# Optimization experiments

Hardware: AMD Instinct MI355X
Metric: run time of the kernel (lower is better)

Reference implementation:

```python
import jax, jax.numpy as jnp
import numpy as np

EPS = 0.1  # eps added to covariance sums, as in torch cov()
N, D, N_CLASSES = 4096, 1024, 64


def setup_inputs() -> dict:
    key = jax.random.key(0)
    k1, k2 = jax.random.split(key)
    inputs = jax.random.normal(k1, (N, D), dtype=jnp.float32)
    targets = jax.random.randint(k2, (N,), 0, N_CLASSES, dtype=jnp.int32)
    return {"inputs": inputs, "targets": targets}


def _masked_sqdiff_sum(M, x):
    # Per-dim sum over masked pairs (i,j) of (x_i - x_j)^2, without
    # materializing the [n, n, d] difference tensor:
    #   sum_ij M_ij (x_id^2 + x_jd^2 - 2 x_id x_jd)
    row = M.sum(axis=1)  # [n]
    col = M.sum(axis=0)  # [n]
    x2 = x * x
    return row @ x2 + col @ x2 - 2.0 * jnp.sum(x * (M @ x), axis=0)  # [d]


def _jeffrey_loss(inputs, targets):
    n = inputs.shape[0]
    same = targets[:, None] == targets[None, :]
    eye = jnp.eye(n, dtype=bool)
    pos_m = (same & ~eye).astype(inputs.dtype)  # positive pairs, i != j
    neg_m = (~same).astype(inputs.dtype)        # negative pairs

    # Covariances are computed on detached diffs in the torch code
    xd = jax.lax.stop_gradient(inputs)
    cnt_pos = pos_m.sum()
    cnt_neg = neg_m.sum()
    sigma1 = (_masked_sqdiff_sum(pos_m, xd) + EPS) / cnt_pos  # [d]
    sigma0 = (_masked_sqdiff_sum(neg_m, xd) + EPS) / cnt_neg  # [d]
    weights = 1.0 / sigma0 - 1.0 / sigma1  # [d], constant w.r.t. grad

    # S[i, j] = sum_d weights_d * (x_i - x_j)_d^2, via gram expansion
    xw = inputs * weights            # [n, d]
    sq = jnp.sum(inputs * xw, axis=1)  # [n], sum_d w_d x_d^2
    S = sq[:, None] + sq[None, :] - 2.0 * inputs @ xw.T  # [n, n]

    # BCEWithLogitsLoss(mean): label 1 on positive pairs (logits a),
    # label 0 on negative pairs (logits b)
    loss_sum = jnp.sum(pos_m * jax.nn.softplus(-S)) + jnp.sum(neg_m * jax.nn.softplus(S))
    return loss_sum / (cnt_pos + cnt_neg)


def reference(inputs, targets):
    return _jeffrey_loss(inputs, targets)
```

## Files before the change

kernel.cpp:

```cpp
#include <hip/hip_runtime.h>
#include <stdint.h>

#define N_ROWS 4096
#define DIM    1024
#define NCLS   64
#define EPSV   0.1f

typedef __attribute__((ext_vector_type(4))) float f32x4;

__device__ __forceinline__ void async_cp16(const void* g, void* l) {
    __builtin_amdgcn_global_load_lds((const __attribute__((address_space(1))) void*)g,
                                     (__attribute__((address_space(3))) void*)l,
                                     16, 0, 0);
}

__device__ __forceinline__ float softplus(float x) {
    return fmaxf(x, 0.f) + __logf(1.f + __expf(-fabsf(x)));
}

__global__ __launch_bounds__(256) void k_cstats(const float* __restrict__ X,
                                                const int* __restrict__ tgt,
                                                float* __restrict__ csumR,
                                                float* __restrict__ csqR) {
    __shared__ int rows[N_ROWS];
    __shared__ int nrows_s;
    int tid = threadIdx.x;
    int c = blockIdx.x >> 2, q = blockIdx.x & 3;
    if (tid == 0) nrows_s = 0;
    __syncthreads();
    for (int i = tid; i < N_ROWS; i += 256)
        if (tgt[i] == c) { int p = atomicAdd(&nrows_s, 1); rows[p] = i; }
    __syncthreads();
    int n = nrows_s;
    int d = q * 256 + tid;
    float s = 0.f, qq = 0.f;
    #pragma unroll 4
    for (int r = 0; r < n; r++) {
        float x = X[(size_t)rows[r] * DIM + d];
        s += x; qq += x * x;
    }
    csumR[c * DIM + d] = s;
    csqR [c * DIM + d] = qq;
}

__global__ __launch_bounds__(1024) void k_weights(const int* __restrict__ tgt,
                                                  const float* __restrict__ csumR,
                                                  const float* __restrict__ csqR,
                                                  float* __restrict__ w,
                                                  float* __restrict__ scal,
                                                  float* __restrict__ loss_out) {
    __shared__ int hist[NCLS];
    __shared__ float redw[16];
    int tid = threadIdx.x;
    if (tid < NCLS) hist[tid] = 0;
    __syncthreads();
    for (int i = tid; i < N_ROWS; i += 1024) atomicAdd(&hist[tgt[i]], 1);
    __syncthreads();
    long long sp = 0, ss = 0;
    for (int c = 0; c < NCLS; c++) { long long cc = hist[c]; sp += cc * (cc - 1); ss += cc * cc; }
    float cnt_pos = (float)sp;
    float cnt_neg = (float)((long long)N_ROWS * N_ROWS - ss);
    int d = tid;
    float A = 0.f, X2 = 0.f, T = 0.f, SS = 0.f;
    #pragma unroll 8
    for (int c = 0; c < NCLS; c++) {
        float s = csumR[c * DIM + d];
        float q = csqR [c * DIM + d];
        A += (float)hist[c] * q; X2 += q; T += s; SS += s * s;
    }
    float posnum = 2.f * (A - SS);
    float negnum = 2.f * ((float)N_ROWS * X2 - A - T * T + SS);
    float wd = cnt_neg / (negnum + EPSV) - cnt_pos / (posnum + EPSV);
    w[d] = wd;
    float m = wd * wd;
    for (int off = 32; off; off >>= 1) m += __shfl_down(m, off, 64);
    int wv = tid >> 6, ln = tid & 63;
    if (ln == 0) redw[wv] = m;
    __syncthreads();
    if (tid == 0) {
        float ms = 0.f;
        #pragma unroll
        for (int i = 0; i < 16; i++) ms += redw[i];
        ms /= 1024.f;
        float sw = exp2f(roundf(log2f(sqrtf(ms) + 1e-30f)));
        scal[0] = sw;
        loss_out[0] = 0.0f;
    }
}

__global__ __launch_bounds__(256) void k_prep(const float* __restrict__ X,
                                              const float* __restrict__ w,
                                              const float* __restrict__ scal,
                                              unsigned int* __restrict__ Xb8,
                                              unsigned int* __restrict__ XWb8,
                                              float* __restrict__ sq) {
    int row = blockIdx.x, tid = threadIdx.x;
    float inv_sw = 1.0f / scal[0];
    float4 x  = ((const float4*)(X + (size_t)row * DIM))[tid];
    float4 ww = ((const float4*)w)[tid];
    float4 xw = make_float4(x.x * ww.x, x.y * ww.y, x.z * ww.z, x.w * ww.w);
    float p = x.x * xw.x + x.y * xw.y + x.z * xw.z + x.w * xw.w;
    unsigned ux = __builtin_amdgcn_cvt_pk_fp8_f32(x.x, x.y, 0, false);
    ux = __builtin_amdgcn_cvt_pk_fp8_f32(x.z, x.w, ux, true);
    unsigned uw = __builtin_amdgcn_cvt_pk_fp8_f32(xw.x * inv_sw, xw.y * inv_sw, 0, false);
    uw = __builtin_amdgcn_cvt_pk_fp8_f32(xw.z * inv_sw, xw.w * inv_sw, uw, true);
    Xb8 [row * 256 + tid] = ux;
    XWb8[row * 256 + tid] = uw;
    for (int off = 32; off; off >>= 1) p += __shfl_down(p, off, 64);
    __shared__ float red[4];
    int wv = tid >> 6, ln = tid & 63;
    if (ln == 0) red[wv] = p;
    __syncthreads();
    if (tid == 0) sq[row] = red[0] + red[1] + red[2] + red[3];
}

__global__ __launch_bounds__(512) void k_gemm_loss(const unsigned char* __restrict__ Xb8,
                                                   const unsigned char* __restrict__ XWb8,
                                                   const float* __restrict__ sq,
                                                   const int* __restrict__ tgt,
                                                   const float* __restrict__ scal,
                                                   float* __restrict__ loss) {
    __shared__ __align__(16) unsigned char As[4][128 * 32];
    __shared__ __align__(16) unsigned char Bs[4][128 * 32];
    __shared__ float sqI[128], sqJ[128];
    __shared__ int   tIs[128], tJs[128];
    __shared__ float red[8];

    int tid = threadIdx.x;
    int wave = tid >> 6, lane = tid & 63;

    int g = blockIdx.x & 7, s = blockIdx.x >> 3;
    int j0 = g, j1 = 15 - g, j2 = 16 + g, j3 = 31 - g;
    int n0 = j0 + 1, n1 = j1 + 1, n2 = j2 + 1;
    int jt, it;
    if      (s < n0)           { jt = j0; it = s; }
    else if (s < n0 + n1)      { jt = j1; it = s - n0; }
    else if (s < n0 + n1 + n2) { jt = j2; it = s - n0 - n1; }
    else                       { jt = j3; it = s - n0 - n1 - n2; }

    bool isA = wave < 4;
    int gIa = wave & 3;
    int r_loc = gIa * 32 + (lane >> 1);
    int swb = ((r_loc >> 1) ^ (r_loc >> 2)) & 1;
    int h_src = (lane & 1) ^ swb;
    int grow = (isA ? it : jt) * 128 + r_loc;
    const unsigned char* gp = (isA ? Xb8 : XWb8) + (size_t)grow * DIM + h_src * 16;
    unsigned char* lbase = (isA ? &As[0][0] : &Bs[0][0]) + gIa * 1024;

    int lr = lane & 15, kq = lane >> 4;
    int offA[4], offB[2];
    int wrow = (wave >> 2) * 64, wcol = (wave & 3) * 32;
    #pragma unroll
    for (int mi = 0; mi < 4; mi++) {
        int row = wrow + mi * 16 + lr;
        offA[mi] = row * 32 + ((kq ^ ((((row >> 1) ^ (row >> 2)) & 1) << 1)) * 8);
    }
    #pragma unroll
    for (int nj = 0; nj < 2; nj++) {
        int col = wcol + nj * 16 + lr;
        offB[nj] = col * 32 + ((kq ^ ((((col >> 1) ^ (col >> 2)) & 1) << 1)) * 8);
    }

    f32x4 acc[4][2];
    #pragma unroll
    for (int i = 0; i < 4; i++)
        #pragma unroll
        for (int j = 0; j < 2; j++) acc[i][j] = (f32x4){0.f, 0.f, 0.f, 0.f};

    #pragma unroll
    for (int st = 0; st < 3; st++) async_cp16(gp + st * 32, lbase + st * (128 * 32));

    for (int kk = 0; kk < 32; kk++) {
        if      (kk < 30)  asm volatile("s_waitcnt vmcnt(2)" ::: "memory");
        else if (kk == 30) asm volatile("s_waitcnt vmcnt(1)" ::: "memory");
        else               asm volatile("s_waitcnt vmcnt(0)" ::: "memory");
        asm volatile("s_barrier" ::: "memory");
        if (kk < 29) {
            async_cp16(gp + (kk + 3) * 32, lbase + ((kk + 3) & 3) * (128 * 32));
        }
        int rd = kk & 3;
        const unsigned char* Ab = As[rd];
        const unsigned char* Bb = Bs[rd];
        long long av[4], bv[2];
        #pragma unroll
        for (int i = 0; i < 4; i++) av[i] = *(const long long*)(Ab + offA[i]);
        #pragma unroll
        for (int j = 0; j < 2; j++) bv[j] = *(const long long*)(Bb + offB[j]);
        #pragma unroll
        for (int i = 0; i < 4; i++)
            #pragma unroll
            for (int j = 0; j < 2; j++)
                acc[i][j] = __builtin_amdgcn_mfma_f32_16x16x32_fp8_fp8(av[i], bv[j], acc[i][j], 0, 0, 0);
    }

    __syncthreads();
    if (tid < 128)      { sqI[tid] = sq[it * 128 + tid]; tIs[tid] = tgt[it * 128 + tid]; }
    else if (tid < 256) { int u = tid - 128; sqJ[u] = sq[jt * 128 + u]; tJs[u] = tgt[jt * 128 + u]; }
    __syncthreads();

    float sw2 = 2.0f * scal[0];
    float sum = 0.f;
    bool diagTile = (it == jt);
    #pragma unroll
    for (int j = 0; j < 2; j++) {
        int col = wcol + j * 16 + (lane & 15);
        float sj = sqJ[col]; int tj = tJs[col];
        #pragma unroll
        for (int i = 0; i < 4; i++) {
            int rbase = wrow + i * 16 + (lane >> 4) * 4;
            #pragma unroll
            for (int r = 0; r < 4; r++) {
                int rowp = rbase + r;
                float S = sqI[rowp] + sj - sw2 * acc[i][j][r];
                float v;
                if (tIs[rowp] == tj) v = (diagTile && rowp == col) ? 0.f : softplus(-S);
                else                 v = softplus(S);
                sum += v;
            }
        }
    }
    float scale = (diagTile ? 1.f : 2.f) * (1.f / ((float)N_ROWS * (float)(N_ROWS - 1)));
    sum *= scale;
    for (int off = 32; off; off >>= 1) sum += __shfl_down(sum, off, 64);
    if (lane == 0) red[wave] = sum;
    __syncthreads();
    if (tid == 0) {
        float t = 0.f;
        #pragma unroll
        for (int wv = 0; wv < 8; wv++) t += red[wv];
        atomicAdd(loss, t);
    }
}

extern "C" void kernel_launch(void* const* d_in, const int* in_sizes, int n_in,
                              void* d_out, int out_size, void* d_ws, size_t ws_size,
                              hipStream_t stream) {
    const float* X  = (const float*)d_in[0];
    const int* tgt  = (const int*)d_in[1];
    float* out = (float*)d_out;
    char* ws = (char*)d_ws;
    const size_t MB = 1u << 20;

    float* w      = (float*)ws;
    float* sq     = (float*)(ws + 4096);
    float* scal   = (float*)(ws + 24576);
    unsigned int* Xb8  = (unsigned int*)(ws + 1 * MB);
    unsigned int* XWb8 = (unsigned int*)(ws + 5 * MB);
    float* csumR  = (float*)(ws + 9 * MB);
    float* csqR   = (float*)(ws + 9 * MB + 256 * 1024);

    k_cstats  <<<256,  256, 0, stream>>>(X, tgt, csumR, csqR);
    k_weights <<<1,   1024, 0, stream>>>(tgt, csumR, csqR, w, scal, out);
    k_prep    <<<4096, 256, 0, stream>>>(X, w, scal, Xb8, XWb8, sq);
    k_gemm_loss<<<528, 512, 0, stream>>>((const unsigned char*)Xb8, (const unsigned char*)XWb8,
                                         sq, tgt, scal, out);
}
```

Baseline: 125.2 us.

## Enlarge per-wave GEMM tile to 64x64 with 256-thread blocks; split weights kernel

The fused fp8 GEMM+loss kernel now runs 4 waves per block instead of 8. Each wave computes a 64x64 sub-tile (4x4 MFMAs), so each LDS fragment load is reused across more MFMAs, and each thread issues two async global-to-LDS copies per stage. The weights kernel is spread over 8 blocks of 128 threads instead of one block of 1024 threads. The fp8 scale factor is now estimated from only the first 128 weight dimensions, which can slightly change the fp8 quantisation range. The GEMM change also raises accumulator register pressure, which may lower occupancy.

```diff
diff --git a/kernel.cpp b/kernel.cpp
--- a/kernel.cpp
+++ b/kernel.cpp
@@ -43,24 +43,24 @@
     csqR [c * DIM + d] = qq;
 }
 
-__global__ __launch_bounds__(1024) void k_weights(const int* __restrict__ tgt,
-                                                  const float* __restrict__ csumR,
-                                                  const float* __restrict__ csqR,
-                                                  float* __restrict__ w,
-                                                  float* __restrict__ scal,
-                                                  float* __restrict__ loss_out) {
+__global__ __launch_bounds__(128) void k_weights(const int* __restrict__ tgt,
+                                                 const float* __restrict__ csumR,
+                                                 const float* __restrict__ csqR,
+                                                 float* __restrict__ w,
+                                                 float* __restrict__ scal,
+                                                 float* __restrict__ loss_out) {
     __shared__ int hist[NCLS];
-    __shared__ float redw[16];
-    int tid = threadIdx.x;
+    __shared__ float redw[2];
+    int tid = threadIdx.x, b = blockIdx.x;
     if (tid < NCLS) hist[tid] = 0;
     __syncthreads();
-    for (int i = tid; i < N_ROWS; i += 1024) atomicAdd(&hist[tgt[i]], 1);
+    for (int i = tid; i < N_ROWS; i += 128) atomicAdd(&hist[tgt[i]], 1);
     __syncthreads();
     long long sp = 0, ss = 0;
     for (int c = 0; c < NCLS; c++) { long long cc = hist[c]; sp += cc * (cc - 1); ss += cc * cc; }
     float cnt_pos = (float)sp;
     float cnt_neg = (float)((long long)N_ROWS * N_ROWS - ss);
-    int d = tid;
+    int d = b * 128 + tid;
     float A = 0.f, X2 = 0.f, T = 0.f, SS = 0.f;
     #pragma unroll 8
     for (int c = 0; c < NCLS; c++) {
@@ -77,13 +77,9 @@
     int wv = tid >> 6, ln = tid & 63;
     if (ln == 0) redw[wv] = m;
     __syncthreads();
-    if (tid == 0) {
-        float ms = 0.f;
-        #pragma unroll
-        for (int i = 0; i < 16; i++) ms += redw[i];
-        ms /= 1024.f;
-        float sw = exp2f(roundf(log2f(sqrtf(ms) + 1e-30f)));
-        scal[0] = sw;
+    if (b == 0 && tid == 0) {
+        float ms = (redw[0] + redw[1]) / 128.f;
+        scal[0] = exp2f(roundf(log2f(sqrtf(ms) + 1e-30f)));
         loss_out[0] = 0.0f;
     }
 }
@@ -114,7 +110,7 @@
     if (tid == 0) sq[row] = red[0] + red[1] + red[2] + red[3];
 }
 
-__global__ __launch_bounds__(512) void k_gemm_loss(const unsigned char* __restrict__ Xb8,
+__global__ __launch_bounds__(256) void k_gemm_loss(const unsigned char* __restrict__ Xb8,
                                                    const unsigned char* __restrict__ XWb8,
                                                    const float* __restrict__ sq,
                                                    const int* __restrict__ tgt,
@@ -124,7 +120,7 @@
     __shared__ __align__(16) unsigned char Bs[4][128 * 32];
     __shared__ float sqI[128], sqJ[128];
     __shared__ int   tIs[128], tJs[128];
-    __shared__ float red[8];
+    __shared__ float red[4];
 
     int tid = threadIdx.x;
     int wave = tid >> 6, lane = tid & 63;
@@ -138,71 +134,81 @@
     else if (s < n0 + n1 + n2) { jt = j2; it = s - n0 - n1; }
     else                       { jt = j3; it = s - n0 - n1 - n2; }
 
-    bool isA = wave < 4;
-    int gIa = wave & 3;
-    int r_loc = gIa * 32 + (lane >> 1);
-    int swb = ((r_loc >> 1) ^ (r_loc >> 2)) & 1;
-    int h_src = (lane & 1) ^ swb;
-    int grow = (isA ? it : jt) * 128 + r_loc;
-    const unsigned char* gp = (isA ? Xb8 : XWb8) + (size_t)grow * DIM + h_src * 16;
-    unsigned char* lbase = (isA ? &As[0][0] : &Bs[0][0]) + gIa * 1024;
+    bool isA = wave < 2;
+    const unsigned char* srcb = (isA ? Xb8 : XWb8) + (size_t)((isA ? it : jt) * 128) * DIM;
+    unsigned char* slab = isA ? &As[0][0] : &Bs[0][0];
+    const unsigned char* gp[2];
+    unsigned char* lb[2];
+    #pragma unroll
+    for (int si = 0; si < 2; si++) {
+        int chunk = (wave & 1) * 128 + si * 64 + lane;
+        int r = chunk >> 1, h = chunk & 1;
+        int swb = ((r >> 1) ^ (r >> 2)) & 1;
+        gp[si] = srcb + (size_t)r * DIM + (h ^ swb) * 16;
+        lb[si] = slab + ((wave & 1) * 128 + si * 64) * 16;
+    }
 
     int lr = lane & 15, kq = lane >> 4;
-    int offA[4], offB[2];
-    int wrow = (wave >> 2) * 64, wcol = (wave & 3) * 32;
+    int offA[4], offB[4];
+    int wrow = (wave >> 1) * 64, wcol = (wave & 1) * 64;
     #pragma unroll
     for (int mi = 0; mi < 4; mi++) {
         int row = wrow + mi * 16 + lr;
-        offA[mi] = row * 32 + ((kq ^ ((((row >> 1) ^ (row >> 2)) & 1) << 1)) * 8);
-    }
-    #pragma unroll
-    for (int nj = 0; nj < 2; nj++) {
-        int col = wcol + nj * 16 + lr;
-        offB[nj] = col * 32 + ((kq ^ ((((col >> 1) ^ (col >> 2)) & 1) << 1)) * 8);
-    }
-
-    f32x4 acc[4][2];
+        int sw = ((row >> 1) ^ (row >> 2)) & 1;
+        offA[mi] = row * 32 + (kq ^ (sw << 1)) * 8;
+        int col = wcol + mi * 16 + lr;
+        int swc = ((col >> 1) ^ (col >> 2)) & 1;
+        offB[mi] = col * 32 + (kq ^ (swc << 1)) * 8;
+    }
+
+    f32x4 acc[4][4];
     #pragma unroll
     for (int i = 0; i < 4; i++)
         #pragma unroll
-        for (int j = 0; j < 2; j++) acc[i][j] = (f32x4){0.f, 0.f, 0.f, 0.f};
-
-    #pragma unroll
-    for (int st = 0; st < 3; st++) async_cp16(gp + st * 32, lbase + st * (128 * 32));
+        for (int j = 0; j < 4; j++) acc[i][j] = (f32x4){0.f, 0.f, 0.f, 0.f};
+
+    #pragma unroll
+    for (int st = 0; st < 3; st++)
+        #pragma unroll
+        for (int si = 0; si < 2; si++)
+            async_cp16(gp[si] + st * 32, lb[si] + st * 4096);
 
     for (int kk = 0; kk < 32; kk++) {
-        if      (kk < 30)  asm volatile("s_waitcnt vmcnt(2)" ::: "memory");
-        else if (kk == 30) asm volatile("s_waitcnt vmcnt(1)" ::: "memory");
+        if      (kk < 30)  asm volatile("s_waitcnt vmcnt(4)" ::: "memory");
+        else if (kk == 30) asm volatile("s_waitcnt vmcnt(2)" ::: "memory");
         else               asm volatile("s_waitcnt vmcnt(0)" ::: "memory");
         asm volatile("s_barrier" ::: "memory");
         if (kk < 29) {
-            async_cp16(gp + (kk + 3) * 32, lbase + ((kk + 3) & 3) * (128 * 32));
+            #pragma unroll
+            for (int si = 0; si < 2; si++)
+                async_cp16(gp[si] + (kk + 3) * 32, lb[si] + ((kk + 3) & 3) * 4096);
         }
         int rd = kk & 3;
         const unsigned char* Ab = As[rd];
         const unsigned char* Bb = Bs[rd];
-        long long av[4], bv[2];
-        #pragma unroll
-        for (int i = 0; i < 4; i++) av[i] = *(const long long*)(Ab + offA[i]);
-        #pragma unroll
-        for (int j = 0; j < 2; j++) bv[j] = *(const long long*)(Bb + offB[j]);
+        long long av[4], bv[4];
+        #pragma unroll
+        for (int i = 0; i < 4; i++) {
+            av[i] = *(const long long*)(Ab + offA[i]);
+            bv[i] = *(const long long*)(Bb + offB[i]);
+        }
         #pragma unroll
         for (int i = 0; i < 4; i++)
             #pragma unroll
-            for (int j = 0; j < 2; j++)
+            for (int j = 0; j < 4; j++)
                 acc[i][j] = __builtin_amdgcn_mfma_f32_16x16x32_fp8_fp8(av[i], bv[j], acc[i][j], 0, 0, 0);
     }
 
     __syncthreads();
-    if (tid < 128)      { sqI[tid] = sq[it * 128 + tid]; tIs[tid] = tgt[it * 128 + tid]; }
-    else if (tid < 256) { int u = tid - 128; sqJ[u] = sq[jt * 128 + u]; tJs[u] = tgt[jt * 128 + u]; }
+    if (tid < 128) { sqI[tid] = sq[it * 128 + tid]; tIs[tid] = tgt[it * 128 + tid]; }
+    else { int u = tid - 128; sqJ[u] = sq[jt * 128 + u]; tJs[u] = tgt[jt * 128 + u]; }
     __syncthreads();
 
     float sw2 = 2.0f * scal[0];
     float sum = 0.f;
     bool diagTile = (it == jt);
     #pragma unroll
-    for (int j = 0; j < 2; j++) {
+    for (int j = 0; j < 4; j++) {
         int col = wcol + j * 16 + (lane & 15);
         float sj = sqJ[col]; int tj = tJs[col];
         #pragma unroll
@@ -224,12 +230,7 @@
     for (int off = 32; off; off >>= 1) sum += __shfl_down(sum, off, 64);
     if (lane == 0) red[wave] = sum;
     __syncthreads();
-    if (tid == 0) {
-        float t = 0.f;
-        #pragma unroll
-        for (int wv = 0; wv < 8; wv++) t += red[wv];
-        atomicAdd(loss, t);
-    }
+    if (tid == 0) atomicAdd(loss, red[0] + red[1] + red[2] + red[3]);
 }
 
 extern "C" void kernel_launch(void* const* d_in, const int* in_sizes, int n_in,
@@ -250,8 +251,8 @@
     float* csqR   = (float*)(ws + 9 * MB + 256 * 1024);
 
     k_cstats  <<<256,  256, 0, stream>>>(X, tgt, csumR, csqR);
-    k_weights <<<1,   1024, 0, stream>>>(tgt, csumR, csqR, w, scal, out);
+    k_weights <<<8,    128, 0, stream>>>(tgt, csumR, csqR, w, scal, out);
     k_prep    <<<4096, 256, 0, stream>>>(X, w, scal, Xb8, XWb8, sq);
-    k_gemm_loss<<<528, 512, 0, stream>>>((const unsigned char*)Xb8, (const unsigned char*)XWb8,
+    k_gemm_loss<<<528, 256, 0, stream>>>((const unsigned char*)Xb8, (const unsigned char*)XWb8,
                                          sq, tgt, scal, out);
 }
```

New measurement: 130.8 us. +4.4%, slower.

## Pre-swizzle fp8 operands in global memory, split weights kernel across blocks

Applied to the files above, without the earlier changes.

The prep kernel now writes the fp8 X and XW rows in an XOR-swizzled chunk order, so the GEMM kernel can copy 16-byte chunks linearly into LDS and use a wider 2-bit XOR swizzle for its fragment reads, reducing LDS bank conflicts. The weights kernel is split from one 1024-thread block into 8 blocks of 128 threads. The scale factor is now computed from only block 0's 128 weights instead of all 1024, which changes the fp8 scaling and may alter accuracy. The GEMM kernel also gets an occupancy hint in its launch bounds.

```diff
diff --git a/kernel.cpp b/kernel.cpp
--- a/kernel.cpp
+++ b/kernel.cpp
@@ -43,24 +43,24 @@
     csqR [c * DIM + d] = qq;
 }
 
-__global__ __launch_bounds__(1024) void k_weights(const int* __restrict__ tgt,
-                                                  const float* __restrict__ csumR,
-                                                  const float* __restrict__ csqR,
-                                                  float* __restrict__ w,
-                                                  float* __restrict__ scal,
-                                                  float* __restrict__ loss_out) {
+__global__ __launch_bounds__(128) void k_weights(const int* __restrict__ tgt,
+                                                 const float* __restrict__ csumR,
+                                                 const float* __restrict__ csqR,
+                                                 float* __restrict__ w,
+                                                 float* __restrict__ scal,
+                                                 float* __restrict__ loss_out) {
     __shared__ int hist[NCLS];
-    __shared__ float redw[16];
-    int tid = threadIdx.x;
+    __shared__ float redw[2];
+    int tid = threadIdx.x, b = blockIdx.x;
     if (tid < NCLS) hist[tid] = 0;
     __syncthreads();
-    for (int i = tid; i < N_ROWS; i += 1024) atomicAdd(&hist[tgt[i]], 1);
+    for (int i = tid; i < N_ROWS; i += 128) atomicAdd(&hist[tgt[i]], 1);
     __syncthreads();
     long long sp = 0, ss = 0;
     for (int c = 0; c < NCLS; c++) { long long cc = hist[c]; sp += cc * (cc - 1); ss += cc * cc; }
     float cnt_pos = (float)sp;
     float cnt_neg = (float)((long long)N_ROWS * N_ROWS - ss);
-    int d = tid;
+    int d = b * 128 + tid;
     float A = 0.f, X2 = 0.f, T = 0.f, SS = 0.f;
     #pragma unroll 8
     for (int c = 0; c < NCLS; c++) {
@@ -77,13 +77,9 @@
     int wv = tid >> 6, ln = tid & 63;
     if (ln == 0) redw[wv] = m;
     __syncthreads();
-    if (tid == 0) {
-        float ms = 0.f;
-        #pragma unroll
-        for (int i = 0; i < 16; i++) ms += redw[i];
-        ms /= 1024.f;
-        float sw = exp2f(roundf(log2f(sqrtf(ms) + 1e-30f)));
-        scal[0] = sw;
+    if (b == 0 && tid == 0) {
+        float ms = (redw[0] + redw[1]) / 128.f;
+        scal[0] = exp2f(roundf(log2f(sqrtf(ms) + 1e-30f)));
         loss_out[0] = 0.0f;
     }
 }
@@ -104,8 +100,11 @@
     ux = __builtin_amdgcn_cvt_pk_fp8_f32(x.z, x.w, ux, true);
     unsigned uw = __builtin_amdgcn_cvt_pk_fp8_f32(xw.x * inv_sw, xw.y * inv_sw, 0, false);
     uw = __builtin_amdgcn_cvt_pk_fp8_f32(xw.z * inv_sw, xw.w * inv_sw, uw, true);
-    Xb8 [row * 256 + tid] = ux;
-    XWb8[row * 256 + tid] = uw;
+    int t = tid >> 3, q = (tid >> 1) & 3, o = tid & 1;
+    int s = (row >> 2) & 3;
+    int widx = row * 256 + t * 8 + (q ^ s) * 2 + o;
+    Xb8 [widx] = ux;
+    XWb8[widx] = uw;
     for (int off = 32; off; off >>= 1) p += __shfl_down(p, off, 64);
     __shared__ float red[4];
     int wv = tid >> 6, ln = tid & 63;
@@ -114,14 +113,14 @@
     if (tid == 0) sq[row] = red[0] + red[1] + red[2] + red[3];
 }
 
-__global__ __launch_bounds__(512) void k_gemm_loss(const unsigned char* __restrict__ Xb8,
-                                                   const unsigned char* __restrict__ XWb8,
-                                                   const float* __restrict__ sq,
-                                                   const int* __restrict__ tgt,
-                                                   const float* __restrict__ scal,
-                                                   float* __restrict__ loss) {
-    __shared__ __align__(16) unsigned char As[4][128 * 32];
-    __shared__ __align__(16) unsigned char Bs[4][128 * 32];
+__global__ __launch_bounds__(512, 4) void k_gemm_loss(const unsigned char* __restrict__ Xb8,
+                                                      const unsigned char* __restrict__ XWb8,
+                                                      const float* __restrict__ sq,
+                                                      const int* __restrict__ tgt,
+                                                      const float* __restrict__ scal,
+                                                      float* __restrict__ loss) {
+    __shared__ __align__(16) unsigned char As[4][4096];
+    __shared__ __align__(16) unsigned char Bs[4][4096];
     __shared__ float sqI[128], sqJ[128];
     __shared__ int   tIs[128], tJs[128];
     __shared__ float red[8];
@@ -130,22 +129,21 @@
     int wave = tid >> 6, lane = tid & 63;
 
     int g = blockIdx.x & 7, s = blockIdx.x >> 3;
-    int j0 = g, j1 = 15 - g, j2 = 16 + g, j3 = 31 - g;
+    int j0 = g, j1 = 15 - g, j2 = 16 + g;
     int n0 = j0 + 1, n1 = j1 + 1, n2 = j2 + 1;
     int jt, it;
     if      (s < n0)           { jt = j0; it = s; }
     else if (s < n0 + n1)      { jt = j1; it = s - n0; }
     else if (s < n0 + n1 + n2) { jt = j2; it = s - n0 - n1; }
-    else                       { jt = j3; it = s - n0 - n1 - n2; }
+    else                       { jt = 31 - g; it = s - n0 - n1 - n2; }
 
     bool isA = wave < 4;
-    int gIa = wave & 3;
-    int r_loc = gIa * 32 + (lane >> 1);
-    int swb = ((r_loc >> 1) ^ (r_loc >> 2)) & 1;
-    int h_src = (lane & 1) ^ swb;
-    int grow = (isA ? it : jt) * 128 + r_loc;
-    const unsigned char* gp = (isA ? Xb8 : XWb8) + (size_t)grow * DIM + h_src * 16;
-    unsigned char* lbase = (isA ? &As[0][0] : &Bs[0][0]) + gIa * 1024;
+    const unsigned char* srcb = (isA ? Xb8 : XWb8) + (size_t)((isA ? it : jt) * 128) * DIM;
+    unsigned char* slab = isA ? &As[0][0] : &Bs[0][0];
+    int ch = (wave & 3) * 64 + lane;
+    int r = ch >> 1, h = ch & 1;
+    const unsigned char* gp = srcb + (size_t)r * DIM + h * 16;
+    unsigned char* lb = slab + (wave & 3) * 1024;
 
     int lr = lane & 15, kq = lane >> 4;
     int offA[4], offB[2];
@@ -153,12 +151,12 @@
     #pragma unroll
     for (int mi = 0; mi < 4; mi++) {
         int row = wrow + mi * 16 + lr;
-        offA[mi] = row * 32 + ((kq ^ ((((row >> 1) ^ (row >> 2)) & 1) << 1)) * 8);
+        offA[mi] = row * 32 + (kq ^ ((row >> 2) & 3)) * 8;
     }
     #pragma unroll
     for (int nj = 0; nj < 2; nj++) {
         int col = wcol + nj * 16 + lr;
-        offB[nj] = col * 32 + ((kq ^ ((((col >> 1) ^ (col >> 2)) & 1) << 1)) * 8);
+        offB[nj] = col * 32 + (kq ^ ((col >> 2) & 3)) * 8;
     }
 
     f32x4 acc[4][2];
@@ -168,16 +166,15 @@
         for (int j = 0; j < 2; j++) acc[i][j] = (f32x4){0.f, 0.f, 0.f, 0.f};
 
     #pragma unroll
-    for (int st = 0; st < 3; st++) async_cp16(gp + st * 32, lbase + st * (128 * 32));
+    for (int st = 0; st < 3; st++) async_cp16(gp + st * 32, lb + st * 4096);
 
     for (int kk = 0; kk < 32; kk++) {
         if      (kk < 30)  asm volatile("s_waitcnt vmcnt(2)" ::: "memory");
         else if (kk == 30) asm volatile("s_waitcnt vmcnt(1)" ::: "memory");
         else               asm volatile("s_waitcnt vmcnt(0)" ::: "memory");
         asm volatile("s_barrier" ::: "memory");
-        if (kk < 29) {
-            async_cp16(gp + (kk + 3) * 32, lbase + ((kk + 3) & 3) * (128 * 32));
-        }
+        if (kk < 29)
+            async_cp16(gp + (kk + 3) * 32, lb + ((kk + 3) & 3) * 4096);
         int rd = kk & 3;
         const unsigned char* Ab = As[rd];
         const unsigned char* Bb = Bs[rd];
@@ -209,9 +206,9 @@
         for (int i = 0; i < 4; i++) {
             int rbase = wrow + i * 16 + (lane >> 4) * 4;
             #pragma unroll
-            for (int r = 0; r < 4; r++) {
-                int rowp = rbase + r;
-                float S = sqI[rowp] + sj - sw2 * acc[i][j][r];
+            for (int rr = 0; rr < 4; rr++) {
+                int rowp = rbase + rr;
+                float S = sqI[rowp] + sj - sw2 * acc[i][j][rr];
                 float v;
                 if (tIs[rowp] == tj) v = (diagTile && rowp == col) ? 0.f : softplus(-S);
                 else                 v = softplus(S);
@@ -250,7 +247,7 @@
     float* csqR   = (float*)(ws + 9 * MB + 256 * 1024);
 
     k_cstats  <<<256,  256, 0, stream>>>(X, tgt, csumR, csqR);
-    k_weights <<<1,   1024, 0, stream>>>(tgt, csumR, csqR, w, scal, out);
+    k_weights <<<8,    128, 0, stream>>>(tgt, csumR, csqR, w, scal, out);
     k_prep    <<<4096, 256, 0, stream>>>(X, w, scal, Xb8, XWb8, sq);
     k_gemm_loss<<<528, 512, 0, stream>>>((const unsigned char*)Xb8, (const unsigned char*)XWb8,
                                          sq, tgt, scal, out);
```

Result: faster. 120.9 us (-3.4%).
